# Kernel tuning notes

Hardware: AMD Instinct MI355X
Metric: run time of the kernel (lower is better)

## Reference

```python
import jax, jax.numpy as jnp
import numpy as np

# Dims: batch B, seq L, embed D, router hidden H, num_blocks NB, top_k K
B, L, D, H, NB, K = 8, 4096, 1024, 64, 16, 2
TEMP = 2.0          # current_temperature buffer (init 2.0), clamp(min=0.1) inert
LN_EPS = 1e-5


def setup_inputs() -> dict:
    key = jax.random.key(0)
    k_x, k_w1, k_w2 = jax.random.split(key, 3)
    return {
        "x": jax.random.normal(k_x, (B, L, D), dtype=jnp.float32),
        "ln_gamma": jnp.ones((D,), dtype=jnp.float32),
        "ln_beta": jnp.zeros((D,), dtype=jnp.float32),
        "W1": jax.random.normal(k_w1, (D, H), dtype=jnp.float32) / np.sqrt(D).astype(np.float32),
        "W2": jax.random.normal(k_w2, (H, NB), dtype=jnp.float32) / np.sqrt(H).astype(np.float32),
    }


def reference(x, ln_gamma, ln_beta, W1, W2):
    # gate: LayerNorm -> Linear(no bias) -> GELU(exact) -> Linear(no bias)
    mu = jnp.mean(x, axis=-1, keepdims=True)
    var = jnp.mean(jnp.square(x - mu), axis=-1, keepdims=True)
    xn = (x - mu) * jax.lax.rsqrt(var + LN_EPS) * ln_gamma + ln_beta
    h = jax.nn.gelu(xn @ W1, approximate=False)          # (B, L, H)
    logits = (h @ W2) / TEMP                              # (B, L, NB)

    probs = jax.nn.softmax(logits, axis=-1)               # (B, L, NB)
    top_probs, indices = jax.lax.top_k(probs, K)          # (B, L, K) each
    weights = top_probs / (jnp.sum(top_probs, axis=-1, keepdims=True) + 1e-8)

    # load-balancing aux loss: f = fraction of assignments per block (detached),
    # P = mean router prob per block
    counts = jnp.zeros((NB,), dtype=probs.dtype).at[indices.reshape(-1)].add(1.0)
    f = jax.lax.stop_gradient(counts) / (B * L * K + 1e-8)
    P = jnp.mean(probs, axis=(0, 1))                      # (NB,)
    aux_loss = NB * jnp.sum(f * P)

    return probs, indices, aux_loss, weights
```

## Files before the change

### kernel.cpp

```cpp
#include <hip/hip_runtime.h>
#include <math.h>

typedef __attribute__((ext_vector_type(8))) short short8;
typedef __attribute__((ext_vector_type(4))) float f32x4;

#define NTOK 32768
#define DDIM 1024
#define HDIM 64
#define NB 16
#define LN_EPS 1e-5f

#define IDX_OFF ((size_t)NTOK * NB)
#define AUX_OFF (IDX_OFF + (size_t)NTOK * 2)
#define WT_OFF  (AUX_OFF + 1)

#define CS_F   64
#define BP_F   4352
#define PART_F 102656

__device__ __forceinline__ short8 as_s8(uint4 u) {
    union { uint4 u; short8 s; } x; x.u = u; return x.s;
}

__device__ __forceinline__ void gld16(const void* g, float* l) {
    __builtin_amdgcn_global_load_lds(
        (const __attribute__((address_space(1))) void*)g,
        (__attribute__((address_space(3))) void*)l, 16, 0, 0);
}

__global__ void pack_kernel(const float* __restrict__ W1,
                            const float* __restrict__ gamma,
                            const float* __restrict__ beta,
                            float* __restrict__ ws) {
    __shared__ float sg[4][64];
    __shared__ float sb[4][64];
    const int s = blockIdx.x;
    const int t = threadIdx.x;

    {
        const int j = t & 63, p = t >> 6;
        float ag = 0.f, ab = 0.f;
        for (int kk = 0; kk < 8; ++kk) {
            const int k = s * 32 + p * 8 + kk;
            const float w = W1[k * HDIM + j];
            ag += gamma[k] * w;
            ab += beta[k] * w;
        }
        sg[p][j] = ag;
        sb[p][j] = ab;
    }

    {
        unsigned int* bp = (unsigned int*)(ws + BP_F);
        const int n = t >> 6;
        const int l = t & 63;
        const int q = l >> 4, c = l & 15;
        const int col = n * 16 + c;
        unsigned int uh[8], um[8], ul[8];
#pragma unroll
        for (int j = 0; j < 8; ++j) {
            const int k = s * 32 + q * 8 + j;
            const float w = gamma[k] * W1[k * HDIM + col];
            const unsigned int hb = __float_as_uint(w) & 0xFFFF0000u;
            const float r = w - __uint_as_float(hb);
            const unsigned int mb = __float_as_uint(r) & 0xFFFF0000u;
            const float r2 = r - __uint_as_float(mb);
            const unsigned int lb = __float_as_uint(r2) & 0xFFFF0000u;
            uh[j] = hb >> 16; um[j] = mb >> 16; ul[j] = lb >> 16;
        }
        const int base = ((s * 4 + n) * 64 + l) * 4;
#pragma unroll
        for (int d = 0; d < 4; ++d) {
            bp[base + d]         = uh[2 * d] | (uh[2 * d + 1] << 16);
            bp[32768 + base + d] = um[2 * d] | (um[2 * d + 1] << 16);
            bp[65536 + base + d] = ul[2 * d] | (ul[2 * d + 1] << 16);
        }
    }
    __syncthreads();
    if (t < 64) {
        atomicAdd(&ws[CS_F + t],      sg[0][t] + sg[1][t] + sg[2][t] + sg[3][t]);
        atomicAdd(&ws[CS_F + 64 + t], sb[0][t] + sb[1][t] + sb[2][t] + sb[3][t]);
    }
}

__device__ __forceinline__ void split8(const f32x4 a0, const f32x4 a1,
                                       short8& AH, short8& AM, short8& AL,
                                       float& s1, float& s2) {
    const float v[8] = {a0.x, a0.y, a0.z, a0.w, a1.x, a1.y, a1.z, a1.w};
    unsigned int ph[4], pm[4], pl[4];
#pragma unroll
    for (int d = 0; d < 4; ++d) {
        const float v0 = v[2 * d], v1 = v[2 * d + 1];
        const unsigned int h0 = __float_as_uint(v0) & 0xFFFF0000u;
        const unsigned int h1 = __float_as_uint(v1) & 0xFFFF0000u;
        const float r0 = v0 - __uint_as_float(h0);
        const float r1 = v1 - __uint_as_float(h1);
        const unsigned int m0 = __float_as_uint(r0) & 0xFFFF0000u;
        const unsigned int m1 = __float_as_uint(r1) & 0xFFFF0000u;
        const float q0 = r0 - __uint_as_float(m0);
        const float q1 = r1 - __uint_as_float(m1);
        ph[d] = (h0 >> 16) | h1;
        pm[d] = (m0 >> 16) | m1;
        pl[d] = (__float_as_uint(q0) >> 16) | (__float_as_uint(q1) & 0xFFFF0000u);
        s1 += v0 + v1;
        s2 = fmaf(v0, v0, fmaf(v1, v1, s2));
    }
    AH = as_s8(make_uint4(ph[0], ph[1], ph[2], ph[3]));
    AM = as_s8(make_uint4(pm[0], pm[1], pm[2], pm[3]));
    AL = as_s8(make_uint4(pl[0], pl[1], pl[2], pl[3]));
}

#define MFMA6(ACC, AH, AM, AL, BH, BM, BL)                                        \
    ACC = __builtin_amdgcn_mfma_f32_16x16x32_bf16(AH, as_s8(BH), ACC, 0, 0, 0);   \
    ACC = __builtin_amdgcn_mfma_f32_16x16x32_bf16(AH, as_s8(BM), ACC, 0, 0, 0);   \
    ACC = __builtin_amdgcn_mfma_f32_16x16x32_bf16(AM, as_s8(BH), ACC, 0, 0, 0);   \
    ACC = __builtin_amdgcn_mfma_f32_16x16x32_bf16(AH, as_s8(BL), ACC, 0, 0, 0);   \
    ACC = __builtin_amdgcn_mfma_f32_16x16x32_bf16(AM, as_s8(BM), ACC, 0, 0, 0);   \
    ACC = __builtin_amdgcn_mfma_f32_16x16x32_bf16(AL, as_s8(BH), ACC, 0, 0, 0);

#define WAITV(N)                                                   \
    asm volatile("s_waitcnt vmcnt(" #N ")" ::: "memory");          \
    __builtin_amdgcn_sched_barrier(0)

#define BARRIER_PUB()                                              \
    asm volatile("s_waitcnt vmcnt(4) lgkmcnt(0)" ::: "memory");    \
    __builtin_amdgcn_s_barrier();                                  \
    asm volatile("" ::: "memory");                                 \
    __builtin_amdgcn_sched_barrier(0)

#define A_F 0
#define B_F 16384
__global__ __launch_bounds__(512, 2)
void router_main(const float* __restrict__ x,
                 const float* __restrict__ ws_ro,
                 const unsigned int* __restrict__ bp,
                 const float* __restrict__ W2,
                 float* __restrict__ part,
                 float* __restrict__ out) {
    __shared__ __align__(16) float smem[28672];
    float* hlds = smem;
    float* w2l  = smem + 8320;
    float* llds = smem + 9344;
    float* cntl = smem + 11904;

    const int t    = threadIdx.x;
    const int wv   = t >> 6;
    const int lane = t & 63;
    const int q = lane >> 4, c = lane & 15;
    const int tok0 = blockIdx.x * 128;
    const int tokw = tok0 + wv * 16;

    float csg[4], csb[4];
#pragma unroll
    for (int n = 0; n < 4; ++n) {
        csg[n] = ws_ro[CS_F + n * 16 + c];
        csb[n] = ws_ro[CS_F + 64 + n * 16 + c];
    }

    const int bidx0 = wv * 3;
    const float* xsrc = x + (size_t)(tokw + c) * DDIM + q * 8;

#define STAGE_B(CI)                                                              \
    {                                                                            \
        float* dst = smem + B_F + ((CI) & 1) * 6144;                             \
        _Pragma("unroll")                                                        \
        for (int i = 0; i < 3; ++i) {                                            \
            const int idx = bidx0 + i;                                           \
            const int st = (idx >= 12) ? 1 : 0;                                  \
            const int rem = idx - st * 12;                                       \
            const int term = rem >> 2, n = rem & 3;                              \
            gld16(bp + term * 32768 + (2 * (CI) + st) * 1024 + n * 256 + lane*4, \
                  dst + st * 3072 + term * 1024 + n * 256);                      \
        }                                                                        \
    }
#define STAGE_A(CI)                                                              \
    {                                                                            \
        float* dst = smem + A_F + ((CI) & 1) * 8192 + wv * 1024;                 \
        const float* src = xsrc + (2 * (CI)) * 32;                               \
        _Pragma("unroll")                                                        \
        for (int j = 0; j < 4; ++j)                                              \
            gld16(src + (j >> 1) * 32 + (j & 1) * 4, dst + j * 256);             \
    }

    STAGE_B(0)
    STAGE_A(0)
    asm volatile("s_waitcnt vmcnt(4)" ::: "memory");
    __builtin_amdgcn_s_barrier();
    asm volatile("" ::: "memory");
    __builtin_amdgcn_sched_barrier(0);

    f32x4 acc[4] = {{0.f,0.f,0.f,0.f},{0.f,0.f,0.f,0.f},{0.f,0.f,0.f,0.f},{0.f,0.f,0.f,0.f}};
    float s1a = 0.f, s2a = 0.f;

#pragma unroll 1
    for (int ci = 0; ci < 16; ++ci) {
        if (ci < 15) {
            STAGE_B(ci + 1)
            STAGE_A(ci + 1)
            WAITV(7);
        } else {
            WAITV(0);
        }
        const float* Ab = smem + A_F + (ci & 1) * 8192 + wv * 1024;
        const float* Bb = smem + B_F + (ci & 1) * 6144;
#pragma unroll
        for (int st = 0; st < 2; ++st) {
            const f32x4 a00 = *(const f32x4*)(Ab + st * 512 + lane * 4);
            const f32x4 a01 = *(const f32x4*)(Ab + st * 512 + 256 + lane * 4);
            short8 AH0, AM0, AL0;
            split8(a00, a01, AH0, AM0, AL0, s1a, s2a);
            const float* Bs = Bb + st * 3072;
#pragma unroll
            for (int n = 0; n < 4; ++n) {
                const uint4 bh = *(const uint4*)(Bs + n * 256 + lane * 4);
                const uint4 bm = *(const uint4*)(Bs + 1024 + n * 256 + lane * 4);
                const uint4 bl = *(const uint4*)(Bs + 2048 + n * 256 + lane * 4);
                MFMA6(acc[n], AH0, AM0, AL0, bh, bm, bl);
            }
        }
        if (ci < 15) {
            BARRIER_PUB();
        }
    }
    __syncthreads();

    s1a += __shfl_xor(s1a, 16, 64); s1a += __shfl_xor(s1a, 32, 64);
    s2a += __shfl_xor(s2a, 16, 64); s2a += __shfl_xor(s2a, 32, 64);

    if (t < 16) cntl[t] = 0.f;
    if (t < 256) *(float4*)(w2l + t * 4) = *(const float4*)(W2 + t * 4);

    {
        float* hw = hlds + wv * 1040;
#pragma unroll
        for (int r = 0; r < 4; ++r) {
            const int tt = q * 4 + r;
            const float S1A = __shfl(s1a, tt, 64), S2A = __shfl(s2a, tt, 64);
            const float muA = S1A * (1.0f / 1024.0f);
            const float rsA = 1.0f / sqrtf(S2A * (1.0f / 1024.0f) - muA * muA + LN_EPS);
#pragma unroll
            for (int n = 0; n < 4; ++n) {
                const float preA = rsA * (acc[n][r] - muA * csg[n]) + csb[n];
                hw[tt * 65 + n * 16 + c] =
                    0.5f * preA * (1.0f + erff(preA * 0.70710678118654752f));
            }
        }
    }
    __syncthreads();

    {
        const int m2 = t >> 2, o = (t & 3) * 4;
        const float* hrow = hlds + (m2 >> 4) * 1040 + (m2 & 15) * 65;
        f32x4 L0 = {0.f, 0.f, 0.f, 0.f};
#pragma unroll 8
        for (int j = 0; j < 64; ++j) {
            L0 += *(const f32x4*)(w2l + j * 16 + o) * hrow[j];
        }
        *(f32x4*)(llds + m2 * 20 + o) = L0 * 0.5f;
    }
    __syncthreads();

    if (t < 128) {
        float p[16];
        float mx = -1e30f;
#pragma unroll
        for (int i = 0; i < NB; ++i) { p[i] = llds[t * 20 + i]; mx = fmaxf(mx, p[i]); }
        float ssum = 0.f;
#pragma unroll
        for (int i = 0; i < NB; ++i) { p[i] = expf(p[i] - mx); ssum += p[i]; }
        const float inv = 1.0f / ssum;
#pragma unroll
        for (int i = 0; i < NB; ++i) { p[i] *= inv; llds[t * 20 + i] = p[i]; }

        float* po = out + (size_t)(tok0 + t) * NB;
#pragma unroll
        for (int u = 0; u < 4; ++u) {
            float4 v; v.x = p[u*4]; v.y = p[u*4+1]; v.z = p[u*4+2]; v.w = p[u*4+3];
            *(float4*)(po + u * 4) = v;
        }

        float b0 = -1.f, b1 = -1.f;
        int i0 = 0, i1 = 0;
#pragma unroll
        for (int i = 0; i < NB; ++i) {
            if (p[i] > b0)      { b1 = b0; i1 = i0; b0 = p[i]; i0 = i; }
            else if (p[i] > b1) { b1 = p[i]; i1 = i; }
        }
        const float wsum = b0 + b1 + 1e-8f;
        out[IDX_OFF + (size_t)(tok0 + t) * 2]     = (float)i0;
        out[IDX_OFF + (size_t)(tok0 + t) * 2 + 1] = (float)i1;
        out[WT_OFF + (size_t)(tok0 + t) * 2]      = b0 / wsum;
        out[WT_OFF + (size_t)(tok0 + t) * 2 + 1]  = b1 / wsum;
        atomicAdd(&cntl[i0], 1.0f);
        atomicAdd(&cntl[i1], 1.0f);
    }
    __syncthreads();

    if (t < 16) {
        float ps = 0.f;
        for (int m = 0; m < 128; ++m) ps += llds[m * 20 + t];
        part[(size_t)blockIdx.x * 32 + t]      = cntl[t];
        part[(size_t)blockIdx.x * 32 + 16 + t] = ps;
    }
}

__global__ void aux_kernel(const float* __restrict__ part,
                           float* __restrict__ gacc,
                           float* __restrict__ out) {
    __shared__ float red[8][32];
    __shared__ float flag;
    const int t = threadIdx.x;
    const int b = blockIdx.x;
    const int i = t & 31, rr = t >> 5;
    const int r0 = b * 16 + rr;
    red[rr][i] = part[(size_t)r0 * 32 + i] + part[(size_t)(r0 + 8) * 32 + i];
    __syncthreads();
    if (t < 32) {
        float tot = 0.f;
#pragma unroll
        for (int p = 0; p < 8; ++p) tot += red[p][t];
        atomicAdd(&gacc[t], tot);
    }
    __syncthreads();
    if (t == 0) {
        __threadfence();
        const unsigned int old = atomicAdd((unsigned int*)(gacc + 32), 1u);
        flag = (old == 15u) ? 1.f : 0.f;
    }
    __syncthreads();
    if (flag != 0.f) {
        if (t < 32) red[0][t] = atomicAdd(&gacc[t], 0.0f);
        __syncthreads();
        if (t == 0) {
            float a = 0.f;
            for (int k = 0; k < NB; ++k) {
                const float f = red[0][k] / (65536.0f + 1e-8f);
                const float P = red[0][16 + k] * (1.0f / 32768.0f);
                a += f * P;
            }
            out[AUX_OFF] = 16.0f * a;
        }
    }
}

extern "C" void kernel_launch(void* const* d_in, const int* in_sizes, int n_in,
                              void* d_out, int out_size, void* d_ws, size_t ws_size,
                              hipStream_t stream) {
    const float* x     = (const float*)d_in[0];
    const float* gamma = (const float*)d_in[1];
    const float* beta  = (const float*)d_in[2];
    const float* W1    = (const float*)d_in[3];
    const float* W2    = (const float*)d_in[4];
    float* out = (float*)d_out;
    float* ws  = (float*)d_ws;

    (void)hipMemsetAsync(ws, 0, 192 * sizeof(float), stream);
    pack_kernel<<<32, 256, 0, stream>>>(W1, gamma, beta, ws);
    router_main<<<NTOK / 128, 512, 0, stream>>>(x, ws, (const unsigned int*)(ws + BP_F),
                                                W2, ws + PART_F, out);
    aux_kernel<<<16, 256, 0, stream>>>(ws + PART_F, ws, out);
}
```

Before: 227.6 us.

## Stage x tiles through registers with nontemporal loads and padded LDS layout

Replaces the direct global-to-LDS async loads of the activation tile with nontemporal global loads into registers. The registers are then written to a padded LDS buffer after the compute step, so each row of a tile is read as coalesced contiguous 16-byte chunks. The nontemporal hint is meant to keep streaming x from polluting cache, and the padding is meant to avoid bank conflicts on the transposed reads. In exchange, each iteration now waits on vmcnt(0) before the barrier instead of allowing partial overlap, the loads use more registers, and the kernel needs more LDS.

Result: faster. 222.6 us (-2.2%).

```diff
diff --git a/kernel.cpp b/kernel.cpp
--- a/kernel.cpp
+++ b/kernel.cpp
@@ -20,6 +20,10 @@
 
 __device__ __forceinline__ short8 as_s8(uint4 u) {
     union { uint4 u; short8 s; } x; x.u = u; return x.s;
+}
+
+__device__ __forceinline__ f32x4 ntload4(const float* p) {
+    return __builtin_nontemporal_load((const f32x4*)p);
 }
 
 __device__ __forceinline__ void gld16(const void* g, float* l) {
@@ -118,18 +122,15 @@
     ACC = __builtin_amdgcn_mfma_f32_16x16x32_bf16(AM, as_s8(BM), ACC, 0, 0, 0);   \
     ACC = __builtin_amdgcn_mfma_f32_16x16x32_bf16(AL, as_s8(BH), ACC, 0, 0, 0);
 
-#define WAITV(N)                                                   \
-    asm volatile("s_waitcnt vmcnt(" #N ")" ::: "memory");          \
+#define PUB()                                                       \
+    asm volatile("s_waitcnt vmcnt(0) lgkmcnt(0)" ::: "memory");     \
+    __builtin_amdgcn_s_barrier();                                   \
     __builtin_amdgcn_sched_barrier(0)
 
-#define BARRIER_PUB()                                              \
-    asm volatile("s_waitcnt vmcnt(4) lgkmcnt(0)" ::: "memory");    \
-    __builtin_amdgcn_s_barrier();                                  \
-    asm volatile("" ::: "memory");                                 \
-    __builtin_amdgcn_sched_barrier(0)
-
 #define A_F 0
-#define B_F 16384
+#define A_BSTRIDE 8704
+#define B_F 17408
+#define B_BSTRIDE 6144
 __global__ __launch_bounds__(512, 2)
 void router_main(const float* __restrict__ x,
                  const float* __restrict__ ws_ro,
@@ -137,7 +138,7 @@
                  const float* __restrict__ W2,
                  float* __restrict__ part,
                  float* __restrict__ out) {
-    __shared__ __align__(16) float smem[28672];
+    __shared__ __align__(16) float smem[29696];
     float* hlds = smem;
     float* w2l  = smem + 8320;
     float* llds = smem + 9344;
@@ -158,11 +159,13 @@
     }
 
     const int bidx0 = wv * 3;
-    const float* xsrc = x + (size_t)(tokw + c) * DDIM + q * 8;
+    const float* xA = x + (size_t)(tokw + q) * DDIM + c * 4;
+    float* awb       = smem + A_F + wv * 1088 + q * 68 + c * 4;
+    const float* arb = smem + A_F + wv * 1088 + c * 68 + q * 8;
 
 #define STAGE_B(CI)                                                              \
     {                                                                            \
-        float* dst = smem + B_F + ((CI) & 1) * 6144;                             \
+        float* dst = smem + B_F + ((CI) & 1) * B_BSTRIDE;                        \
         _Pragma("unroll")                                                        \
         for (int i = 0; i < 3; ++i) {                                            \
             const int idx = bidx0 + i;                                           \
@@ -175,51 +178,61 @@
     }
 #define STAGE_A(CI)                                                              \
     {                                                                            \
-        float* dst = smem + A_F + ((CI) & 1) * 8192 + wv * 1024;                 \
-        const float* src = xsrc + (2 * (CI)) * 32;                               \
+        const float* srcA = xA + (CI) * 64;                                      \
+        ar0 = ntload4(srcA);                                                     \
+        ar1 = ntload4(srcA + 4096);                                              \
+        ar2 = ntload4(srcA + 8192);                                              \
+        ar3 = ntload4(srcA + 12288);                                             \
+    }
+#define DS_WRITE_A(CI)                                                           \
+    {                                                                            \
+        float* dw = awb + ((CI) & 1) * A_BSTRIDE;                                \
+        *(f32x4*)(dw)       = ar0;                                               \
+        *(f32x4*)(dw + 272) = ar1;                                               \
+        *(f32x4*)(dw + 544) = ar2;                                               \
+        *(f32x4*)(dw + 816) = ar3;                                               \
+    }
+#define COMPUTE(CI)                                                              \
+    {                                                                            \
+        const float* Ab = arb + ((CI) & 1) * A_BSTRIDE;                          \
+        const float* Bb = smem + B_F + ((CI) & 1) * B_BSTRIDE;                   \
         _Pragma("unroll")                                                        \
-        for (int j = 0; j < 4; ++j)                                              \
-            gld16(src + (j >> 1) * 32 + (j & 1) * 4, dst + j * 256);             \
-    }
-
-    STAGE_B(0)
-    STAGE_A(0)
-    asm volatile("s_waitcnt vmcnt(4)" ::: "memory");
-    __builtin_amdgcn_s_barrier();
-    asm volatile("" ::: "memory");
-    __builtin_amdgcn_sched_barrier(0);
+        for (int st = 0; st < 2; ++st) {                                         \
+            const f32x4 a00 = *(const f32x4*)(Ab + st * 32);                     \
+            const f32x4 a01 = *(const f32x4*)(Ab + st * 32 + 4);                 \
+            short8 AH0, AM0, AL0;                                                \
+            split8(a00, a01, AH0, AM0, AL0, s1a, s2a);                           \
+            const float* Bs = Bb + st * 3072;                                    \
+            _Pragma("unroll")                                                    \
+            for (int n = 0; n < 4; ++n) {                                        \
+                const uint4 bh = *(const uint4*)(Bs + n * 256 + lane * 4);       \
+                const uint4 bm = *(const uint4*)(Bs + 1024 + n * 256 + lane*4);  \
+                const uint4 bl = *(const uint4*)(Bs + 2048 + n * 256 + lane*4);  \
+                MFMA6(acc[n], AH0, AM0, AL0, bh, bm, bl);                        \
+            }                                                                    \
+        }                                                                        \
+    }
 
     f32x4 acc[4] = {{0.f,0.f,0.f,0.f},{0.f,0.f,0.f,0.f},{0.f,0.f,0.f,0.f},{0.f,0.f,0.f,0.f}};
     float s1a = 0.f, s2a = 0.f;
+    f32x4 ar0, ar1, ar2, ar3;
+
+    STAGE_A(0)
+    STAGE_B(0)
+    DS_WRITE_A(0)
+    PUB();
 
 #pragma unroll 1
     for (int ci = 0; ci < 16; ++ci) {
         if (ci < 15) {
+            STAGE_A(ci + 1)
             STAGE_B(ci + 1)
-            STAGE_A(ci + 1)
-            WAITV(7);
-        } else {
-            WAITV(0);
-        }
-        const float* Ab = smem + A_F + (ci & 1) * 8192 + wv * 1024;
-        const float* Bb = smem + B_F + (ci & 1) * 6144;
-#pragma unroll
-        for (int st = 0; st < 2; ++st) {
-            const f32x4 a00 = *(const f32x4*)(Ab + st * 512 + lane * 4);
-            const f32x4 a01 = *(const f32x4*)(Ab + st * 512 + 256 + lane * 4);
-            short8 AH0, AM0, AL0;
-            split8(a00, a01, AH0, AM0, AL0, s1a, s2a);
-            const float* Bs = Bb + st * 3072;
-#pragma unroll
-            for (int n = 0; n < 4; ++n) {
-                const uint4 bh = *(const uint4*)(Bs + n * 256 + lane * 4);
-                const uint4 bm = *(const uint4*)(Bs + 1024 + n * 256 + lane * 4);
-                const uint4 bl = *(const uint4*)(Bs + 2048 + n * 256 + lane * 4);
-                MFMA6(acc[n], AH0, AM0, AL0, bh, bm, bl);
-            }
-        }
+            __builtin_amdgcn_sched_barrier(0);
+        }
+        COMPUTE(ci)
         if (ci < 15) {
-            BARRIER_PUB();
+            DS_WRITE_A(ci + 1)
+            PUB();
         }
     }
     __syncthreads();
```
